# Kernel optimization log

Measured on AMD Instinct MI355X. Metric: run time of the kernel, lower is better.

## Reference

```python
import jax, jax.numpy as jnp
import numpy as np

N_NODES = 50000
N_EDGES = 600000
FEAT = 128
HID = 128
OUT = 64
N_LAYERS = 4
N_GRAPHS = 128
BN_EPS = 1e-5


def setup_inputs() -> dict:
    key = jax.random.key(0)
    ks = jax.random.split(key, 16)
    x = jax.random.normal(ks[0], (N_NODES, FEAT), dtype=jnp.float32)
    edge_index = jax.random.randint(ks[1], (2, N_EDGES), 0, N_NODES, dtype=jnp.int32)
    batch = jnp.sort(jax.random.randint(ks[2], (N_NODES,), 0, N_GRAPHS, dtype=jnp.int32))
    s = 1.0 / np.sqrt(HID)
    # feat_dim == hidden_dim so all per-layer MLP weights stack to [L, HID, HID]
    W1 = jax.random.normal(ks[3], (N_LAYERS, HID, HID), dtype=jnp.float32) * s
    b1 = jnp.zeros((N_LAYERS, HID), dtype=jnp.float32)
    W2 = jax.random.normal(ks[4], (N_LAYERS, HID, HID), dtype=jnp.float32) * s
    b2 = jnp.zeros((N_LAYERS, HID), dtype=jnp.float32)
    gamma = jnp.ones((N_LAYERS, HID), dtype=jnp.float32)
    beta = jnp.zeros((N_LAYERS, HID), dtype=jnp.float32)
    Wf1 = jax.random.normal(ks[5], (HID, HID), dtype=jnp.float32) * s
    bf1 = jnp.zeros((HID,), dtype=jnp.float32)
    Wf2 = jax.random.normal(ks[6], (HID, OUT), dtype=jnp.float32) * s
    bf2 = jnp.zeros((OUT,), dtype=jnp.float32)
    return {"x": x, "edge_index": edge_index, "batch": batch,
            "W1": W1, "b1": b1, "W2": W2, "b2": b2,
            "gamma": gamma, "beta": beta,
            "Wf1": Wf1, "bf1": bf1, "Wf2": Wf2, "bf2": bf2}


def reference(x, edge_index, batch, W1, b1, W2, b2, gamma, beta, Wf1, bf1, Wf2, bf2):
    src, dst = edge_index[0], edge_index[1]
    h = x
    for l in range(N_LAYERS):
        # GINConv (eps=0): h_i <- MLP(h_i + sum_{j in N(i)} h_j)
        agg = jax.ops.segment_sum(h[src], dst, num_segments=N_NODES)
        h = h + agg
        h = jnp.matmul(jax.nn.relu(jnp.matmul(h, W1[l]) + b1[l]), W2[l]) + b2[l]
        # BatchNorm1d (training mode: batch stats over node dim)
        mean = jnp.mean(h, axis=0)
        var = jnp.var(h, axis=0)
        h = (h - mean) * jax.lax.rsqrt(var + BN_EPS) * gamma[l] + beta[l]
        h = jax.nn.relu(h)
    # global_add_pool over graph ids
    g = jax.ops.segment_sum(h, batch, num_segments=N_GRAPHS)  # [G, HID]
    out = jnp.matmul(jax.nn.relu(jnp.matmul(g, Wf1) + bf1), Wf2) + bf2  # [G, OUT]
    return out
```

## Files before the change

kernel.cpp:

```cpp
#include <hip/hip_runtime.h>

#define NN 50000
#define NE 600000
#define HD 128
#define OUTF 64
#define NL 4
#define NG 128
#define BN_EPS 1e-5f
#define NSB 196

typedef __attribute__((ext_vector_type(8))) short short8v;
typedef __attribute__((ext_vector_type(4))) float float4v;

#define LDSW 136

__device__ inline unsigned short f2bf(float f) {
    unsigned int u = __float_as_uint(f);
    return (unsigned short)((u + 0x7FFF + ((u >> 16) & 1)) >> 16);
}
__device__ inline float bf2f(short s) {
    return __uint_as_float(((unsigned int)(unsigned short)s) << 16);
}

__global__ __launch_bounds__(256) void pack_w_kernel(
    const float* __restrict__ W1, const float* __restrict__ W2,
    short* __restrict__ wpack, float* __restrict__ stats4)
{
    int gid = blockIdx.x * 256 + threadIdx.x;
    if (gid < 256)
        reinterpret_cast<float4*>(stats4)[gid] = (float4){0.f, 0.f, 0.f, 0.f};
    int l  = gid & 63;
    int kb = (gid >> 6) & 3;
    int nt = (gid >> 8) & 7;
    int w  = gid >> 11;
    const float* W = (w & 1) ? (W2 + (size_t)(w >> 1) * HD * HD)
                             : (W1 + (size_t)(w >> 1) * HD * HD);
    int col  = nt * 16 + (l & 15);
    int krow = kb * 32 + (l >> 4) * 8;
    short* o = wpack + (size_t)w * 16384 + ((size_t)(nt * 4 + kb) * 64 + l) * 8;
    #pragma unroll
    for (int i = 0; i < 8; i++)
        o[i] = (short)f2bf(W[(size_t)(krow + i) * HD + col]);
}

__global__ __launch_bounds__(256) void cvt_bf16_kernel(
    const float* __restrict__ x, short* __restrict__ hb)
{
    int idx = blockIdx.x * 256 + threadIdx.x;
    if (idx >= NN * 32) return;
    float4 v = reinterpret_cast<const float4*>(x)[idx];
    short4 o = make_short4((short)f2bf(v.x), (short)f2bf(v.y),
                           (short)f2bf(v.z), (short)f2bf(v.w));
    reinterpret_cast<short4*>(hb)[idx] = o;
}

template<bool BN>
__global__ __launch_bounds__(512) void layer_kernel(
    const short* __restrict__ inb, const float* __restrict__ stats_prev,
    const float* __restrict__ gamma_p, const float* __restrict__ beta_p,
    const int* __restrict__ row_ptr, const int* __restrict__ csr,
    const short* __restrict__ wp1, const float* __restrict__ b1,
    const short* __restrict__ wp2, const float* __restrict__ b2,
    short* __restrict__ Cb, float* __restrict__ sums, float* __restrict__ sumsq)
{
    __shared__ __align__(16) short As[64 * LDSW];
    __shared__ float sscale[HD];
    __shared__ float sshift[HD];
    const int t = threadIdx.x;
    const int row0 = blockIdx.x * 64;

    float sc[8], sh[8];
    const int c8 = (t & 15) * 8;
    if (BN) {
        if (t < HD) {
            const float invN = 1.f / (float)NN;
            float mean = stats_prev[t] * invN;
            float var = stats_prev[HD + t] * invN - mean * mean;
            float inv = rsqrtf(var + BN_EPS);
            float s = gamma_p[t] * inv;
            sscale[t] = s;
            sshift[t] = beta_p[t] - mean * s;
        }
        __syncthreads();
        #pragma unroll
        for (int i = 0; i < 8; i++) { sc[i] = sscale[c8 + i]; sh[i] = sshift[c8 + i]; }
    }

    {
        const int ng = t >> 4;
        #pragma unroll
        for (int it = 0; it < 2; it++) {
            int lr = it * 32 + ng;
            int n = row0 + lr;
            float acc[8] = {0, 0, 0, 0, 0, 0, 0, 0};
            if (n < NN) {
                short8v s = *reinterpret_cast<const short8v*>(&inb[(size_t)n * HD + c8]);
                #pragma unroll
                for (int i = 0; i < 8; i++)
                    acc[i] = BN ? fmaxf(bf2f(s[i]) * sc[i] + sh[i], 0.f) : bf2f(s[i]);
                int p = row_ptr[n], pe = row_ptr[n + 1];
                for (; p + 2 <= pe; p += 2) {
                    int s0 = csr[p], s1 = csr[p + 1];
                    short8v a = *reinterpret_cast<const short8v*>(&inb[(size_t)s0 * HD + c8]);
                    short8v b = *reinterpret_cast<const short8v*>(&inb[(size_t)s1 * HD + c8]);
                    if (BN) {
                        #pragma unroll
                        for (int i = 0; i < 8; i++)
                            acc[i] += fmaxf(bf2f(a[i]) * sc[i] + sh[i], 0.f)
                                    + fmaxf(bf2f(b[i]) * sc[i] + sh[i], 0.f);
                    } else {
                        #pragma unroll
                        for (int i = 0; i < 8; i++) acc[i] += bf2f(a[i]) + bf2f(b[i]);
                    }
                }
                if (p < pe) {
                    short8v a = *reinterpret_cast<const short8v*>(&inb[(size_t)csr[p] * HD + c8]);
                    #pragma unroll
                    for (int i = 0; i < 8; i++)
                        acc[i] += BN ? fmaxf(bf2f(a[i]) * sc[i] + sh[i], 0.f) : bf2f(a[i]);
                }
            }
            short8v o;
            #pragma unroll
            for (int i = 0; i < 8; i++) o[i] = (short)f2bf(acc[i]);
            *reinterpret_cast<short8v*>(&As[lr * LDSW + c8]) = o;
        }
    }
    __syncthreads();

    const int wv = t >> 6, l = t & 63;
    const int l16 = l & 15, lhi = l >> 4;
    const int wrow = (wv >> 1) * 16;
    const int nc0 = (wv & 1) * 4;

    short8v a[4];
    #pragma unroll
    for (int kb = 0; kb < 4; kb++)
        a[kb] = *reinterpret_cast<const short8v*>(&As[(wrow + l16) * LDSW + kb * 32 + lhi * 8]);
    __syncthreads();

    float4v acc[4];
    #pragma unroll
    for (int q = 0; q < 4; q++) acc[q] = (float4v){0.f, 0.f, 0.f, 0.f};
    {
        const short8v* wp = reinterpret_cast<const short8v*>(wp1);
        #pragma unroll
        for (int q = 0; q < 4; q++) {
            int nt = nc0 + q;
            #pragma unroll
            for (int kb = 0; kb < 4; kb++) {
                short8v b = wp[(nt * 4 + kb) * 64 + l];
                acc[q] = __builtin_amdgcn_mfma_f32_16x16x32_bf16(a[kb], b, acc[q], 0, 0, 0);
            }
        }
    }
    #pragma unroll
    for (int q = 0; q < 4; q++) {
        int nt = nc0 + q;
        float bnt = b1[nt * 16 + l16];
        #pragma unroll
        for (int j = 0; j < 4; j++) {
            float v = fmaxf(acc[q][j] + bnt, 0.f);
            As[(wrow + lhi * 4 + j) * LDSW + nt * 16 + l16] = (short)f2bf(v);
        }
    }
    __syncthreads();

    #pragma unroll
    for (int kb = 0; kb < 4; kb++)
        a[kb] = *reinterpret_cast<const short8v*>(&As[(wrow + l16) * LDSW + kb * 32 + lhi * 8]);

    #pragma unroll
    for (int q = 0; q < 4; q++) acc[q] = (float4v){0.f, 0.f, 0.f, 0.f};
    {
        const short8v* wp = reinterpret_cast<const short8v*>(wp2);
        #pragma unroll
        for (int q = 0; q < 4; q++) {
            int nt = nc0 + q;
            #pragma unroll
            for (int kb = 0; kb < 4; kb++) {
                short8v b = wp[(nt * 4 + kb) * 64 + l];
                acc[q] = __builtin_amdgcn_mfma_f32_16x16x32_bf16(a[kb], b, acc[q], 0, 0, 0);
            }
        }
    }

    __syncthreads();
    float* redS = reinterpret_cast<float*>(As);
    float* redQ = redS + 4 * HD;
    #pragma unroll
    for (int q = 0; q < 4; q++) {
        int nt = nc0 + q;
        float bnt = b2[nt * 16 + l16];
        float snt = 0.f, qnt = 0.f;
        #pragma unroll
        for (int j = 0; j < 4; j++) {
            int r = row0 + wrow + lhi * 4 + j;
            if (r < NN) {
                float v = acc[q][j] + bnt;
                Cb[(size_t)r * HD + nt * 16 + l16] = (short)f2bf(v);
                snt += v; qnt += v * v;
            }
        }
        snt += __shfl_xor(snt, 16); snt += __shfl_xor(snt, 32);
        qnt += __shfl_xor(qnt, 16); qnt += __shfl_xor(qnt, 32);
        if (lhi == 0) {
            redS[(wv >> 1) * HD + nt * 16 + l16] = snt;
            redQ[(wv >> 1) * HD + nt * 16 + l16] = qnt;
        }
    }
    __syncthreads();
    if (t < HD) {
        float ss = redS[0 * HD + t] + redS[1 * HD + t] + redS[2 * HD + t] + redS[3 * HD + t];
        float qq = redQ[0 * HD + t] + redQ[1 * HD + t] + redQ[2 * HD + t] + redQ[3 * HD + t];
        atomicAdd(&sums[t], ss);
        atomicAdd(&sumsq[t], qq);
    }
}

__global__ __launch_bounds__(256) void deg_hist_kernel(
    const int* __restrict__ dst, int* __restrict__ deg)
{
    int e = blockIdx.x * 256 + threadIdx.x;
    if (e < NE) atomicAdd(&deg[dst[e]], 1);
}

__global__ __launch_bounds__(256) void scan_partial_kernel(
    const int* __restrict__ deg, int* __restrict__ bsum)
{
    __shared__ int sd[256];
    int t = threadIdx.x;
    int i = blockIdx.x * 256 + t;
    sd[t] = (i < NN) ? deg[i] : 0;
    __syncthreads();
    for (int o = 128; o > 0; o >>= 1) {
        if (t < o) sd[t] += sd[t + o];
        __syncthreads();
    }
    if (t == 0) bsum[blockIdx.x] = sd[0];
}

__global__ __launch_bounds__(256) void scan_bsums_kernel(
    const int* __restrict__ bsum, int* __restrict__ boff)
{
    __shared__ int sd[256];
    int t = threadIdx.x;
    int v = (t < NSB) ? bsum[t] : 0;
    sd[t] = v;
    __syncthreads();
    for (int o = 1; o < 256; o <<= 1) {
        int x = (t >= o) ? sd[t - o] : 0;
        __syncthreads();
        sd[t] += x;
        __syncthreads();
    }
    if (t < NSB) boff[t] = sd[t] - v;
}

__global__ __launch_bounds__(256) void scan_final_kernel(
    const int* __restrict__ deg, const int* __restrict__ boff,
    int* __restrict__ row_ptr, int* __restrict__ cursor)
{
    __shared__ int sd[256];
    int t = threadIdx.x;
    int i = blockIdx.x * 256 + t;
    int v = (i < NN) ? deg[i] : 0;
    sd[t] = v;
    __syncthreads();
    for (int o = 1; o < 256; o <<= 1) {
        int x = (t >= o) ? sd[t - o] : 0;
        __syncthreads();
        sd[t] += x;
        __syncthreads();
    }
    int excl = sd[t] - v + boff[blockIdx.x];
    if (i < NN) { row_ptr[i] = excl; cursor[i] = excl; }
    if (i == NN - 1) row_ptr[NN] = excl + v;
}

__global__ __launch_bounds__(256) void fill_csr_kernel(
    const int* __restrict__ src, const int* __restrict__ dst,
    int* __restrict__ cursor, int* __restrict__ csr)
{
    int e = blockIdx.x * 256 + threadIdx.x;
    if (e >= NE) return;
    int p = atomicAdd(&cursor[dst[e]], 1);
    csr[p] = src[e];
}

__global__ __launch_bounds__(256) void pool_kernel_v4(
    const short* __restrict__ Cb, const float* __restrict__ stats,
    const float* __restrict__ gamma_p, const float* __restrict__ beta_p,
    const int* __restrict__ batch, float* __restrict__ g)
{
    __shared__ float sscale[HD];
    __shared__ float sshift[HD];
    const int t = threadIdx.x;
    if (t < HD) {
        const float invN = 1.f / (float)NN;
        float mean = stats[t] * invN;
        float var = stats[HD + t] * invN - mean * mean;
        float inv = rsqrtf(var + BN_EPS);
        float s = gamma_p[t] * inv;
        sscale[t] = s;
        sshift[t] = beta_p[t] - mean * s;
    }
    __syncthreads();

    const int gr = blockIdx.x;
    int lo = 0, hi = NN;
    while (lo < hi) { int m = (lo + hi) >> 1; if (batch[m] < gr) lo = m + 1; else hi = m; }
    const int start = lo;
    hi = NN;
    while (lo < hi) { int m = (lo + hi) >> 1; if (batch[m] <= gr) lo = m + 1; else hi = m; }
    const int end = lo;

    const int cg = t & 15;
    const int rg = t >> 4;
    float sc[8], sh[8];
    #pragma unroll
    for (int i = 0; i < 8; i++) { sc[i] = sscale[cg * 8 + i]; sh[i] = sshift[cg * 8 + i]; }

    float acc[8] = {0, 0, 0, 0, 0, 0, 0, 0};
    for (int r = start + rg; r < end; r += 16) {
        short8v v = *reinterpret_cast<const short8v*>(&Cb[(size_t)r * HD + cg * 8]);
        #pragma unroll
        for (int i = 0; i < 8; i++)
            acc[i] += fmaxf(bf2f(v[i]) * sc[i] + sh[i], 0.f);
    }
    __shared__ float red[16][HD];
    #pragma unroll
    for (int i = 0; i < 8; i++) red[rg][cg * 8 + i] = acc[i];
    __syncthreads();
    if (t < HD) {
        float s = 0.f;
        #pragma unroll
        for (int k = 0; k < 16; k++) s += red[k][t];
        g[gr * HD + t] = s;
    }
}

__global__ __launch_bounds__(128) void final_kernel(
    const float* __restrict__ g, const float* __restrict__ Wf1,
    const float* __restrict__ bf1, const float* __restrict__ Wf2,
    const float* __restrict__ bf2, float* __restrict__ out)
{
    __shared__ float gr[HD];
    __shared__ float yr[HD];
    int r = blockIdx.x, c = threadIdx.x;
    gr[c] = g[r * HD + c];
    __syncthreads();
    float acc = bf1[c];
    for (int k = 0; k < HD; k++) acc += gr[k] * Wf1[k * HD + c];
    yr[c] = fmaxf(acc, 0.f);
    __syncthreads();
    if (c < OUTF) {
        float o = bf2[c];
        for (int k = 0; k < HD; k++) o += yr[k] * Wf2[k * OUTF + c];
        out[r * OUTF + c] = o;
    }
}

extern "C" void kernel_launch(void* const* d_in, const int* in_sizes, int n_in,
                              void* d_out, int out_size, void* d_ws, size_t ws_size,
                              hipStream_t stream)
{
    const float* x     = (const float*)d_in[0];
    const int*   ei    = (const int*)  d_in[1];
    const int*   batch = (const int*)  d_in[2];
    const float* W1    = (const float*)d_in[3];
    const float* b1    = (const float*)d_in[4];
    const float* W2    = (const float*)d_in[5];
    const float* b2    = (const float*)d_in[6];
    const float* gamma = (const float*)d_in[7];
    const float* beta  = (const float*)d_in[8];
    const float* Wf1   = (const float*)d_in[9];
    const float* bf1   = (const float*)d_in[10];
    const float* Wf2   = (const float*)d_in[11];
    const float* bf2   = (const float*)d_in[12];
    float* out = (float*)d_out;

    float* ws   = (float*)d_ws;
    const size_t BIG = (size_t)NN * HD;
    short* hb  = (short*)ws;
    short* CbA = (short*)ws + BIG;
    short* CbB = (short*)ws + 2 * BIG;
    float* smal = ws + 3 * BIG;
    float* stats4 = smal;
    float* gpool  = smal + 2048;
    int* ip      = (int*)(smal + 65536);
    int* deg     = ip;
    int* row_ptr = ip + NN;
    int* cursor  = row_ptr + NN + 1;
    int* bsum    = cursor + NN;
    int* boff    = bsum + 256;
    int* csr     = boff + 256;
    short* wpack = (short*)(csr + NE);

    const int* src = ei;
    const int* dst = ei + NE;

    const int layer_grid = (NN + 63) / 64;
    const int cvt_grid  = (NN * 32 + 255) / 256;
    const int edge_grid = (NE + 255) / 256;

    pack_w_kernel<<<64, 256, 0, stream>>>(W1, W2, wpack, stats4);
    cvt_bf16_kernel<<<cvt_grid, 256, 0, stream>>>(x, hb);
    hipMemsetAsync(deg, 0, NN * sizeof(int), stream);
    deg_hist_kernel<<<edge_grid, 256, 0, stream>>>(dst, deg);
    scan_partial_kernel<<<NSB, 256, 0, stream>>>(deg, bsum);
    scan_bsums_kernel<<<1, 256, 0, stream>>>(bsum, boff);
    scan_final_kernel<<<NSB, 256, 0, stream>>>(deg, boff, row_ptr, cursor);
    fill_csr_kernel<<<edge_grid, 256, 0, stream>>>(src, dst, cursor, csr);

    const short* lin[NL + 1] = {hb, CbA, CbB, CbA, CbB};
    for (int l = 0; l < NL; l++) {
        float* sums = stats4 + l * 256;
        if (l == 0) {
            layer_kernel<false><<<layer_grid, 512, 0, stream>>>(
                lin[0], nullptr, nullptr, nullptr, row_ptr, csr,
                wpack + 0 * 16384, b1,
                wpack + 1 * 16384, b2,
                (short*)lin[1], sums, sums + 128);
        } else {
            layer_kernel<true><<<layer_grid, 512, 0, stream>>>(
                lin[l], stats4 + (l - 1) * 256, gamma + (l - 1) * HD, beta + (l - 1) * HD,
                row_ptr, csr,
                wpack + (size_t)(l * 2 + 0) * 16384, b1 + l * HD,
                wpack + (size_t)(l * 2 + 1) * 16384, b2 + l * HD,
                (short*)lin[l + 1], sums, sums + 128);
        }
    }

    pool_kernel_v4<<<NG, 256, 0, stream>>>(
        lin[NL], stats4 + 3 * 256, gamma + 3 * HD, beta + 3 * HD, batch, gpool);
    final_kernel<<<NG, 128, 0, stream>>>(gpool, Wf1, bf1, Wf2, bf2, out);
}
```

Before: 305.8 us.

## Shrink layer tile to 48 rows, merge scan, pool/final kernels and deg memset

Layer kernel tile drops from 64 to 48 rows, giving more blocks and better CU balance at the cost of 2 of 8 waves idling in the MFMA phase. The three-kernel CSR scan is replaced by a single-block 1024-thread scan. Pooling is fused with the final MLP, and the degree memset is folded into the weight-pack kernel. Together these cut launch count and tail imbalance, but the single-block scan is serial and the wasted waves reduce MFMA efficiency.

```diff
diff --git a/kernel.cpp b/kernel.cpp
--- a/kernel.cpp
+++ b/kernel.cpp
@@ -7,12 +7,12 @@
 #define NL 4
 #define NG 128
 #define BN_EPS 1e-5f
-#define NSB 196
 
 typedef __attribute__((ext_vector_type(8))) short short8v;
 typedef __attribute__((ext_vector_type(4))) float float4v;
 
 #define LDSW 136
+#define TR 48
 
 __device__ inline unsigned short f2bf(float f) {
     unsigned int u = __float_as_uint(f);
@@ -24,11 +24,13 @@
 
 __global__ __launch_bounds__(256) void pack_w_kernel(
     const float* __restrict__ W1, const float* __restrict__ W2,
-    short* __restrict__ wpack, float* __restrict__ stats4)
+    short* __restrict__ wpack, float* __restrict__ stats4, int* __restrict__ deg)
 {
     int gid = blockIdx.x * 256 + threadIdx.x;
     if (gid < 256)
         reinterpret_cast<float4*>(stats4)[gid] = (float4){0.f, 0.f, 0.f, 0.f};
+    if (gid < 12500)
+        reinterpret_cast<int4*>(deg)[gid] = (int4){0, 0, 0, 0};
     int l  = gid & 63;
     int kb = (gid >> 6) & 3;
     int nt = (gid >> 8) & 7;
@@ -63,11 +65,11 @@
     const short* __restrict__ wp2, const float* __restrict__ b2,
     short* __restrict__ Cb, float* __restrict__ sums, float* __restrict__ sumsq)
 {
-    __shared__ __align__(16) short As[64 * LDSW];
+    __shared__ __align__(16) short As[TR * LDSW];
     __shared__ float sscale[HD];
     __shared__ float sshift[HD];
     const int t = threadIdx.x;
-    const int row0 = blockIdx.x * 64;
+    const int row0 = blockIdx.x * TR;
 
     float sc[8], sh[8];
     const int c8 = (t & 15) * 8;
@@ -91,39 +93,41 @@
         #pragma unroll
         for (int it = 0; it < 2; it++) {
             int lr = it * 32 + ng;
-            int n = row0 + lr;
-            float acc[8] = {0, 0, 0, 0, 0, 0, 0, 0};
-            if (n < NN) {
-                short8v s = *reinterpret_cast<const short8v*>(&inb[(size_t)n * HD + c8]);
-                #pragma unroll
-                for (int i = 0; i < 8; i++)
-                    acc[i] = BN ? fmaxf(bf2f(s[i]) * sc[i] + sh[i], 0.f) : bf2f(s[i]);
-                int p = row_ptr[n], pe = row_ptr[n + 1];
-                for (; p + 2 <= pe; p += 2) {
-                    int s0 = csr[p], s1 = csr[p + 1];
-                    short8v a = *reinterpret_cast<const short8v*>(&inb[(size_t)s0 * HD + c8]);
-                    short8v b = *reinterpret_cast<const short8v*>(&inb[(size_t)s1 * HD + c8]);
-                    if (BN) {
+            if (lr < TR) {
+                int n = row0 + lr;
+                float acc[8] = {0, 0, 0, 0, 0, 0, 0, 0};
+                if (n < NN) {
+                    short8v s = *reinterpret_cast<const short8v*>(&inb[(size_t)n * HD + c8]);
+                    #pragma unroll
+                    for (int i = 0; i < 8; i++)
+                        acc[i] = BN ? fmaxf(bf2f(s[i]) * sc[i] + sh[i], 0.f) : bf2f(s[i]);
+                    int p = row_ptr[n], pe = row_ptr[n + 1];
+                    for (; p + 2 <= pe; p += 2) {
+                        int s0 = csr[p], s1 = csr[p + 1];
+                        short8v a = *reinterpret_cast<const short8v*>(&inb[(size_t)s0 * HD + c8]);
+                        short8v b = *reinterpret_cast<const short8v*>(&inb[(size_t)s1 * HD + c8]);
+                        if (BN) {
+                            #pragma unroll
+                            for (int i = 0; i < 8; i++)
+                                acc[i] += fmaxf(bf2f(a[i]) * sc[i] + sh[i], 0.f)
+                                        + fmaxf(bf2f(b[i]) * sc[i] + sh[i], 0.f);
+                        } else {
+                            #pragma unroll
+                            for (int i = 0; i < 8; i++) acc[i] += bf2f(a[i]) + bf2f(b[i]);
+                        }
+                    }
+                    if (p < pe) {
+                        short8v a = *reinterpret_cast<const short8v*>(&inb[(size_t)csr[p] * HD + c8]);
                         #pragma unroll
                         for (int i = 0; i < 8; i++)
-                            acc[i] += fmaxf(bf2f(a[i]) * sc[i] + sh[i], 0.f)
-                                    + fmaxf(bf2f(b[i]) * sc[i] + sh[i], 0.f);
-                    } else {
-                        #pragma unroll
-                        for (int i = 0; i < 8; i++) acc[i] += bf2f(a[i]) + bf2f(b[i]);
+                            acc[i] += BN ? fmaxf(bf2f(a[i]) * sc[i] + sh[i], 0.f) : bf2f(a[i]);
                     }
                 }
-                if (p < pe) {
-                    short8v a = *reinterpret_cast<const short8v*>(&inb[(size_t)csr[p] * HD + c8]);
-                    #pragma unroll
-                    for (int i = 0; i < 8; i++)
-                        acc[i] += BN ? fmaxf(bf2f(a[i]) * sc[i] + sh[i], 0.f) : bf2f(a[i]);
-                }
-            }
-            short8v o;
-            #pragma unroll
-            for (int i = 0; i < 8; i++) o[i] = (short)f2bf(acc[i]);
-            *reinterpret_cast<short8v*>(&As[lr * LDSW + c8]) = o;
+                short8v o;
+                #pragma unroll
+                for (int i = 0; i < 8; i++) o[i] = (short)f2bf(acc[i]);
+                *reinterpret_cast<short8v*>(&As[lr * LDSW + c8]) = o;
+            }
         }
     }
     __syncthreads();
@@ -132,17 +136,20 @@
     const int l16 = l & 15, lhi = l >> 4;
     const int wrow = (wv >> 1) * 16;
     const int nc0 = (wv & 1) * 4;
+    const bool act = (wv < 6);
 
     short8v a[4];
-    #pragma unroll
-    for (int kb = 0; kb < 4; kb++)
-        a[kb] = *reinterpret_cast<const short8v*>(&As[(wrow + l16) * LDSW + kb * 32 + lhi * 8]);
+    if (act) {
+        #pragma unroll
+        for (int kb = 0; kb < 4; kb++)
+            a[kb] = *reinterpret_cast<const short8v*>(&As[(wrow + l16) * LDSW + kb * 32 + lhi * 8]);
+    }
     __syncthreads();
 
     float4v acc[4];
     #pragma unroll
     for (int q = 0; q < 4; q++) acc[q] = (float4v){0.f, 0.f, 0.f, 0.f};
-    {
+    if (act) {
         const short8v* wp = reinterpret_cast<const short8v*>(wp1);
         #pragma unroll
         for (int q = 0; q < 4; q++) {
@@ -153,26 +160,25 @@
                 acc[q] = __builtin_amdgcn_mfma_f32_16x16x32_bf16(a[kb], b, acc[q], 0, 0, 0);
             }
         }
-    }
-    #pragma unroll
-    for (int q = 0; q < 4; q++) {
-        int nt = nc0 + q;
-        float bnt = b1[nt * 16 + l16];
-        #pragma unroll
-        for (int j = 0; j < 4; j++) {
-            float v = fmaxf(acc[q][j] + bnt, 0.f);
-            As[(wrow + lhi * 4 + j) * LDSW + nt * 16 + l16] = (short)f2bf(v);
-        }
-    }
-    __syncthreads();
-
-    #pragma unroll
-    for (int kb = 0; kb < 4; kb++)
-        a[kb] = *reinterpret_cast<const short8v*>(&As[(wrow + l16) * LDSW + kb * 32 + lhi * 8]);
-
-    #pragma unroll
-    for (int q = 0; q < 4; q++) acc[q] = (float4v){0.f, 0.f, 0.f, 0.f};
-    {
+        #pragma unroll
+        for (int q = 0; q < 4; q++) {
+            int nt = nc0 + q;
+            float bnt = b1[nt * 16 + l16];
+            #pragma unroll
+            for (int j = 0; j < 4; j++) {
+                float v = fmaxf(acc[q][j] + bnt, 0.f);
+                As[(wrow + lhi * 4 + j) * LDSW + nt * 16 + l16] = (short)f2bf(v);
+            }
+        }
+    }
+    __syncthreads();
+
+    if (act) {
+        #pragma unroll
+        for (int kb = 0; kb < 4; kb++)
+            a[kb] = *reinterpret_cast<const short8v*>(&As[(wrow + l16) * LDSW + kb * 32 + lhi * 8]);
+        #pragma unroll
+        for (int q = 0; q < 4; q++) acc[q] = (float4v){0.f, 0.f, 0.f, 0.f};
         const short8v* wp = reinterpret_cast<const short8v*>(wp2);
         #pragma unroll
         for (int q = 0; q < 4; q++) {
@@ -187,32 +193,34 @@
 
     __syncthreads();
     float* redS = reinterpret_cast<float*>(As);
-    float* redQ = redS + 4 * HD;
-    #pragma unroll
-    for (int q = 0; q < 4; q++) {
-        int nt = nc0 + q;
-        float bnt = b2[nt * 16 + l16];
-        float snt = 0.f, qnt = 0.f;
-        #pragma unroll
-        for (int j = 0; j < 4; j++) {
-            int r = row0 + wrow + lhi * 4 + j;
-            if (r < NN) {
-                float v = acc[q][j] + bnt;
-                Cb[(size_t)r * HD + nt * 16 + l16] = (short)f2bf(v);
-                snt += v; qnt += v * v;
-            }
-        }
-        snt += __shfl_xor(snt, 16); snt += __shfl_xor(snt, 32);
-        qnt += __shfl_xor(qnt, 16); qnt += __shfl_xor(qnt, 32);
-        if (lhi == 0) {
-            redS[(wv >> 1) * HD + nt * 16 + l16] = snt;
-            redQ[(wv >> 1) * HD + nt * 16 + l16] = qnt;
+    float* redQ = redS + 3 * HD;
+    if (act) {
+        #pragma unroll
+        for (int q = 0; q < 4; q++) {
+            int nt = nc0 + q;
+            float bnt = b2[nt * 16 + l16];
+            float snt = 0.f, qnt = 0.f;
+            #pragma unroll
+            for (int j = 0; j < 4; j++) {
+                int r = row0 + wrow + lhi * 4 + j;
+                if (r < NN) {
+                    float v = acc[q][j] + bnt;
+                    Cb[(size_t)r * HD + nt * 16 + l16] = (short)f2bf(v);
+                    snt += v; qnt += v * v;
+                }
+            }
+            snt += __shfl_xor(snt, 16); snt += __shfl_xor(snt, 32);
+            qnt += __shfl_xor(qnt, 16); qnt += __shfl_xor(qnt, 32);
+            if (lhi == 0) {
+                redS[(wv >> 1) * HD + nt * 16 + l16] = snt;
+                redQ[(wv >> 1) * HD + nt * 16 + l16] = qnt;
+            }
         }
     }
     __syncthreads();
     if (t < HD) {
-        float ss = redS[0 * HD + t] + redS[1 * HD + t] + redS[2 * HD + t] + redS[3 * HD + t];
-        float qq = redQ[0 * HD + t] + redQ[1 * HD + t] + redQ[2 * HD + t] + redQ[3 * HD + t];
+        float ss = redS[0 * HD + t] + redS[1 * HD + t] + redS[2 * HD + t];
+        float qq = redQ[0 * HD + t] + redQ[1 * HD + t] + redQ[2 * HD + t];
         atomicAdd(&sums[t], ss);
         atomicAdd(&sumsq[t], qq);
     }
@@ -225,57 +233,36 @@
     if (e < NE) atomicAdd(&deg[dst[e]], 1);
 }
 
-__global__ __launch_bounds__(256) void scan_partial_kernel(
-    const int* __restrict__ deg, int* __restrict__ bsum)
-{
-    __shared__ int sd[256];
-    int t = threadIdx.x;
-    int i = blockIdx.x * 256 + t;
-    sd[t] = (i < NN) ? deg[i] : 0;
-    __syncthreads();
-    for (int o = 128; o > 0; o >>= 1) {
-        if (t < o) sd[t] += sd[t + o];
+__global__ __launch_bounds__(1024) void scan_kernel(
+    const int* __restrict__ deg, int* __restrict__ row_ptr, int* __restrict__ cursor)
+{
+    __shared__ int sums[1024];
+    const int t = threadIdx.x;
+    const int CH = (NN + 1023) / 1024;
+    const int base = t * CH;
+    int s = 0;
+    for (int i = 0; i < CH; i++) {
+        int idx = base + i;
+        if (idx < NN) s += deg[idx];
+    }
+    sums[t] = s;
+    __syncthreads();
+    int v = s;
+    for (int o = 1; o < 1024; o <<= 1) {
+        int x = (t >= o) ? sums[t - o] : 0;
         __syncthreads();
-    }
-    if (t == 0) bsum[blockIdx.x] = sd[0];
-}
-
-__global__ __launch_bounds__(256) void scan_bsums_kernel(
-    const int* __restrict__ bsum, int* __restrict__ boff)
-{
-    __shared__ int sd[256];
-    int t = threadIdx.x;
-    int v = (t < NSB) ? bsum[t] : 0;
-    sd[t] = v;
-    __syncthreads();
-    for (int o = 1; o < 256; o <<= 1) {
-        int x = (t >= o) ? sd[t - o] : 0;
+        sums[t] += x;
         __syncthreads();
-        sd[t] += x;
-        __syncthreads();
-    }
-    if (t < NSB) boff[t] = sd[t] - v;
-}
-
-__global__ __launch_bounds__(256) void scan_final_kernel(
-    const int* __restrict__ deg, const int* __restrict__ boff,
-    int* __restrict__ row_ptr, int* __restrict__ cursor)
-{
-    __shared__ int sd[256];
-    int t = threadIdx.x;
-    int i = blockIdx.x * 256 + t;
-    int v = (i < NN) ? deg[i] : 0;
-    sd[t] = v;
-    __syncthreads();
-    for (int o = 1; o < 256; o <<= 1) {
-        int x = (t >= o) ? sd[t - o] : 0;
-        __syncthreads();
-        sd[t] += x;
-        __syncthreads();
-    }
-    int excl = sd[t] - v + boff[blockIdx.x];
-    if (i < NN) { row_ptr[i] = excl; cursor[i] = excl; }
-    if (i == NN - 1) row_ptr[NN] = excl + v;
+    }
+    int run = sums[t] - v;
+    for (int i = 0; i < CH; i++) {
+        int idx = base + i;
+        if (idx < NN) {
+            row_ptr[idx] = run; cursor[idx] = run;
+            run += deg[idx];
+        }
+    }
+    if (t == 1023) row_ptr[NN] = run;
 }
 
 __global__ __launch_bounds__(256) void fill_csr_kernel(
@@ -288,13 +275,18 @@
     csr[p] = src[e];
 }
 
-__global__ __launch_bounds__(256) void pool_kernel_v4(
+__global__ __launch_bounds__(256) void pool_final_kernel(
     const short* __restrict__ Cb, const float* __restrict__ stats,
     const float* __restrict__ gamma_p, const float* __restrict__ beta_p,
-    const int* __restrict__ batch, float* __restrict__ g)
+    const int* __restrict__ batch, const float* __restrict__ Wf1,
+    const float* __restrict__ bf1, const float* __restrict__ Wf2,
+    const float* __restrict__ bf2, float* __restrict__ out)
 {
     __shared__ float sscale[HD];
     __shared__ float sshift[HD];
+    __shared__ float red[16][HD];
+    __shared__ float gr[HD];
+    __shared__ float yr[HD];
     const int t = threadIdx.x;
     if (t < HD) {
         const float invN = 1.f / (float)NN;
@@ -307,12 +299,12 @@
     }
     __syncthreads();
 
-    const int gr = blockIdx.x;
+    const int g = blockIdx.x;
     int lo = 0, hi = NN;
-    while (lo < hi) { int m = (lo + hi) >> 1; if (batch[m] < gr) lo = m + 1; else hi = m; }
+    while (lo < hi) { int m = (lo + hi) >> 1; if (batch[m] < g) lo = m + 1; else hi = m; }
     const int start = lo;
     hi = NN;
-    while (lo < hi) { int m = (lo + hi) >> 1; if (batch[m] <= gr) lo = m + 1; else hi = m; }
+    while (lo < hi) { int m = (lo + hi) >> 1; if (batch[m] <= g) lo = m + 1; else hi = m; }
     const int end = lo;
 
     const int cg = t & 15;
@@ -328,7 +320,6 @@
         for (int i = 0; i < 8; i++)
             acc[i] += fmaxf(bf2f(v[i]) * sc[i] + sh[i], 0.f);
     }
-    __shared__ float red[16][HD];
     #pragma unroll
     for (int i = 0; i < 8; i++) red[rg][cg * 8 + i] = acc[i];
     __syncthreads();
@@ -336,28 +327,19 @@
         float s = 0.f;
         #pragma unroll
         for (int k = 0; k < 16; k++) s += red[k][t];
-        g[gr * HD + t] = s;
-    }
-}
-
-__global__ __launch_bounds__(128) void final_kernel(
-    const float* __restrict__ g, const float* __restrict__ Wf1,
-    const float* __restrict__ bf1, const float* __restrict__ Wf2,
-    const float* __restrict__ bf2, float* __restrict__ out)
-{
-    __shared__ float gr[HD];
-    __shared__ float yr[HD];
-    int r = blockIdx.x, c = threadIdx.x;
-    gr[c] = g[r * HD + c];
-    __syncthreads();
-    float acc = bf1[c];
-    for (int k = 0; k < HD; k++) acc += gr[k] * Wf1[k * HD + c];
-    yr[c] = fmaxf(acc, 0.f);
-    __syncthreads();
-    if (c < OUTF) {
-        float o = bf2[c];
-        for (int k = 0; k < HD; k++) o += yr[k] * Wf2[k * OUTF + c];
-        out[r * OUTF + c] = o;
+        gr[t] = s;
+    }
+    __syncthreads();
+    if (t < HD) {
+        float a = bf1[t];
+        for (int k = 0; k < HD; k++) a += gr[k] * Wf1[k * HD + t];
+        yr[t] = fmaxf(a, 0.f);
+    }
+    __syncthreads();
+    if (t < OUTF) {
+        float o = bf2[t];
+        for (int k = 0; k < HD; k++) o += yr[k] * Wf2[k * OUTF + t];
+        out[g * OUTF + t] = o;
     }
 }
 
@@ -387,30 +369,24 @@
     short* CbB = (short*)ws + 2 * BIG;
     float* smal = ws + 3 * BIG;
     float* stats4 = smal;
-    float* gpool  = smal + 2048;
     int* ip      = (int*)(smal + 65536);
     int* deg     = ip;
     int* row_ptr = ip + NN;
     int* cursor  = row_ptr + NN + 1;
-    int* bsum    = cursor + NN;
-    int* boff    = bsum + 256;
-    int* csr     = boff + 256;
+    int* csr     = cursor + NN;
     short* wpack = (short*)(csr + NE);
 
     const int* src = ei;
     const int* dst = ei + NE;
 
-    const int layer_grid = (NN + 63) / 64;
+    const int layer_grid = (NN + TR - 1) / TR;
     const int cvt_grid  = (NN * 32 + 255) / 256;
     const int edge_grid = (NE + 255) / 256;
 
-    pack_w_kernel<<<64, 256, 0, stream>>>(W1, W2, wpack, stats4);
+    pack_w_kernel<<<64, 256, 0, stream>>>(W1, W2, wpack, stats4, deg);
     cvt_bf16_kernel<<<cvt_grid, 256, 0, stream>>>(x, hb);
-    hipMemsetAsync(deg, 0, NN * sizeof(int), stream);
     deg_hist_kernel<<<edge_grid, 256, 0, stream>>>(dst, deg);
-    scan_partial_kernel<<<NSB, 256, 0, stream>>>(deg, bsum);
-    scan_bsums_kernel<<<1, 256, 0, stream>>>(bsum, boff);
-    scan_final_kernel<<<NSB, 256, 0, stream>>>(deg, boff, row_ptr, cursor);
+    scan_kernel<<<1, 1024, 0, stream>>>(deg, row_ptr, cursor);
     fill_csr_kernel<<<edge_grid, 256, 0, stream>>>(src, dst, cursor, csr);
 
     const short* lin[NL + 1] = {hb, CbA, CbB, CbA, CbB};
@@ -432,7 +408,7 @@
         }
     }
 
-    pool_kernel_v4<<<NG, 256, 0, stream>>>(
-        lin[NL], stats4 + 3 * 256, gamma + 3 * HD, beta + 3 * HD, batch, gpool);
-    final_kernel<<<NG, 128, 0, stream>>>(gpool, Wf1, bf1, Wf2, bf2, out);
-}
+    pool_final_kernel<<<NG, 256, 0, stream>>>(
+        lin[NL], stats4 + 3 * 256, gamma + 3 * HD, beta + 3 * HD, batch,
+        Wf1, bf1, Wf2, bf2, out);
+}
```

New measurement: 493.7 us. 61.4% more time.
